# Performance work log

Measured on AMD Instinct MI355X. Metric: run time of the kernel, lower is better.

## Reference

```python
import jax, jax.numpy as jnp
import numpy as np

N_EMBED = 1024
N_HEAD = 16
SEQ = 2048
BATCH = 2


def setup_inputs() -> dict:
    key = jax.random.key(0)
    ks = jax.random.split(key, 5)
    scale_in = 1.0 / np.sqrt(N_EMBED)
    x = jax.random.normal(ks[0], (BATCH, SEQ, N_EMBED), dtype=jnp.float32)
    # attn_proj: Linear(n_embed, 3*n_embed); stored as [in, out] so y = x @ W + b
    W_qkv = jax.random.normal(ks[1], (N_EMBED, 3 * N_EMBED), dtype=jnp.float32) * scale_in
    b_qkv = jax.random.normal(ks[2], (3 * N_EMBED,), dtype=jnp.float32) * 0.01
    # fin_proj: Linear(n_embed, n_embed)
    W_out = jax.random.normal(ks[3], (N_EMBED, N_EMBED), dtype=jnp.float32) * scale_in
    b_out = jax.random.normal(ks[4], (N_EMBED,), dtype=jnp.float32) * 0.01
    return {"x": x, "W_qkv": W_qkv, "b_qkv": b_qkv, "W_out": W_out, "b_out": b_out}


def reference(x, W_qkv, b_qkv, W_out, b_out):
    B, S, D = x.shape
    H = N_HEAD
    hd = D // H
    qkv = x @ W_qkv + b_qkv  # [B, S, 3D]
    q, k, v = jnp.split(qkv, 3, axis=-1)
    # [B, H, S, hd]
    q = q.reshape(B, S, H, hd).transpose(0, 2, 1, 3)
    k = k.reshape(B, S, H, hd).transpose(0, 2, 1, 3)
    v = v.reshape(B, S, H, hd).transpose(0, 2, 1, 3)
    scores = jnp.einsum("bhqd,bhkd->bhqk", q, k) * (1.0 / np.sqrt(hd))
    causal = jnp.tril(jnp.ones((S, S), dtype=bool))  # lower-triangular mask
    scores = jnp.where(causal[None, None], scores, -jnp.inf)
    probs = jax.nn.softmax(scores, axis=-1)
    # dropout is identity in eval mode (inference reference)
    attn = jnp.einsum("bhqk,bhkd->bhqd", probs, v)  # [B, H, S, hd]
    attn = attn.transpose(0, 2, 1, 3).reshape(B, S, D)
    return attn @ W_out + b_out
```

## Files before the change

### kernel.cpp

```cpp
#include <hip/hip_runtime.h>

typedef short bf16x8 __attribute__((ext_vector_type(8)));
typedef short bf16x4 __attribute__((ext_vector_type(4)));
typedef float f32x4 __attribute__((ext_vector_type(4)));
typedef int i32x4 __attribute__((ext_vector_type(4)));
typedef int i32x2 __attribute__((ext_vector_type(2)));

#define MFMA16x16x32(a, b, c) __builtin_amdgcn_mfma_f32_16x16x32_bf16(a, b, c, 0, 0, 0)
#define TRR(dst, a) asm volatile("ds_read_b64_tr_b16 %0, %1" : "=v"(dst) : "v"(a))

__device__ __forceinline__ unsigned short f2bf(float f) {
  union { float f; unsigned u; } v; v.f = f;
  unsigned u = v.u + 0x7FFFu + ((v.u >> 16) & 1u);
  return (unsigned short)(u >> 16);
}

__device__ __forceinline__ unsigned cvtpk(float lo, float hi) {
  unsigned r;
  asm("v_cvt_pk_bf16_f32 %0, %1, %2" : "=v"(r) : "v"(lo), "v"(hi));
  return r;
}

__device__ __forceinline__ float max3f(float a, float b, float c) {
  float d;
  asm("v_max3_f32 %0, %1, %2, %3" : "=v"(d) : "v"(a), "v"(b), "v"(c));
  return d;
}

__device__ __forceinline__ void gload16(const void* g, void* l) {
  __builtin_amdgcn_global_load_lds((const __attribute__((address_space(1))) void*)g,
                                   (__attribute__((address_space(3))) void*)l, 16, 0, 0);
}

__device__ __forceinline__ unsigned ldsoff(const void* p) {
  return (unsigned)(unsigned long long)(const __attribute__((address_space(3))) void*)p;
}

__global__ __launch_bounds__(256) void conv_bf16(const float* __restrict__ in,
                                                 unsigned short* __restrict__ out, int n8) {
  int i = blockIdx.x * 256 + threadIdx.x;
  if (i >= n8) return;
  const float4* p = reinterpret_cast<const float4*>(in + (long)i * 8);
  float4 a = p[0], b = p[1];
  i32x4 o;
  o[0] = cvtpk(a.x, a.y); o[1] = cvtpk(a.z, a.w);
  o[2] = cvtpk(b.x, b.y); o[3] = cvtpk(b.z, b.w);
  *reinterpret_cast<i32x4*>(out + (long)i * 8) = o;
}

__global__ __launch_bounds__(256) void trans_f32_bf16(const float* __restrict__ W,
                                                      unsigned short* __restrict__ Wt,
                                                      int K, int N) {
  __shared__ float tile[32][33];
  int n0 = blockIdx.x << 5, k0 = blockIdx.y << 5;
  int tx = threadIdx.x, ty = threadIdx.y;
#pragma unroll
  for (int i = 0; i < 32; i += 8)
    tile[ty + i][tx] = W[(long)(k0 + ty + i) * N + n0 + tx];
  __syncthreads();
#pragma unroll
  for (int i = 0; i < 32; i += 8)
    Wt[(long)(n0 + ty + i) * K + k0 + tx] = f2bf(tile[tx][ty + i]);
}

template <int BF16OUT>
__global__ __launch_bounds__(256) void gemm_bt(const unsigned short* __restrict__ A,
                                               const unsigned short* __restrict__ Bt,
                                               const float* __restrict__ bias,
                                               void* __restrict__ Cv,
                                               int M, int N, int K) {
  __shared__ __align__(128) unsigned short As[8192];
  __shared__ __align__(128) unsigned short Bs[8192];
  int t = threadIdx.x;
  int w = t >> 6, l = t & 63;
  int g = l >> 4, m16 = l & 15;
  int wr = w >> 1, wc = w & 1;
  int nwg = gridDim.x * gridDim.y;
  int f = blockIdx.y * gridDim.x + blockIdx.x;
  int q8 = nwg >> 3;
  int s = (f & 7) * q8 + (f >> 3);
  int bx = s % gridDim.x, by = s / gridDim.x;
  long am0 = (long)by << 7;
  long bn0 = (long)bx << 7;
  f32x4 acc[4][4];
#pragma unroll
  for (int i = 0; i < 4; ++i)
#pragma unroll
    for (int j = 0; j < 4; ++j) acc[i][j] = (f32x4){0.f, 0.f, 0.f, 0.f};

  for (int k0 = 0; k0 < K; k0 += 64) {
#pragma unroll
    for (int i = 0; i < 4; ++i) {
      int seg = i * 4 + w;
      int flat = (seg << 9) + (l << 3);
      int r_ = flat >> 6, c_ = flat & 63;
      gload16(A + (am0 + r_) * K + k0 + c_, &As[seg << 9]);
      gload16(Bt + (bn0 + r_) * K + k0 + c_, &Bs[seg << 9]);
    }
    asm volatile("s_waitcnt vmcnt(0)" ::: "memory");
    __syncthreads();
#pragma unroll
    for (int kk = 0; kk < 2; ++kk) {
      bf16x8 af[4], bfr[4];
#pragma unroll
      for (int im = 0; im < 4; ++im)
        af[im] = *(const bf16x8*)&As[((wr << 6) + (im << 4) + m16) * 64 + (kk << 5) + (g << 3)];
#pragma unroll
      for (int in = 0; in < 4; ++in)
        bfr[in] = *(const bf16x8*)&Bs[((wc << 6) + (in << 4) + m16) * 64 + (kk << 5) + (g << 3)];
      __builtin_amdgcn_s_setprio(1);
#pragma unroll
      for (int im = 0; im < 4; ++im)
#pragma unroll
        for (int in = 0; in < 4; ++in)
          acc[im][in] = MFMA16x16x32(af[im], bfr[in], acc[im][in]);
      __builtin_amdgcn_s_setprio(0);
    }
    __syncthreads();
  }

#pragma unroll
  for (int im = 0; im < 4; ++im) {
#pragma unroll
    for (int in = 0; in < 4; ++in) {
      long col = bn0 + (wc << 6) + (in << 4) + m16;
      float bval = bias[col];
#pragma unroll
      for (int r = 0; r < 4; ++r) {
        long row = am0 + (wr << 6) + (im << 4) + (g << 2) + r;
        float v = acc[im][in][r] + bval;
        if (BF16OUT)
          ((unsigned short*)Cv)[row * N + col] = f2bf(v);
        else
          ((float*)Cv)[row * N + col] = v;
      }
    }
  }
}

__global__ __launch_bounds__(256, 3) void attn_fwd(const unsigned short* __restrict__ qkv,
                                                   unsigned short* __restrict__ out) {
  const int D3 = 3072;
  const float C1 = 0.18033688f;
  const float THR = 11.5415603f;
  __shared__ __align__(128) unsigned short Ks[8192];
  __shared__ __align__(128) unsigned short Vs[8192];
  int b = blockIdx.x >> 4, h = blockIdx.x & 15;
  int yy = blockIdx.y;
  int qt = (yy & 1) ? (31 - (yy >> 1)) : (yy >> 1);
  int t = threadIdx.x;
  int w = t >> 6, l = t & 63;
  int g = l >> 4, m16 = l & 15;
  long base = (long)b * 2048 * D3;
  const unsigned short* kbase = qkv + base + 1024 + h * 64;
  const unsigned short* vbase = qkv + base + 2048 + h * 64;

  int l8 = l >> 3, sc = l & 7;
  int kof = (w * 8 + l8) * D3 + ((sc ^ l8) << 3);
  int vof = ((w * 8 + l8) * 4 + (sc >> 1)) * D3 + ((sc & 1) << 3);
  const f32x4 zero4 = (f32x4){0.f, 0.f, 0.f, 0.f};

  int qrow = (qt << 6) + (w << 4) + m16;
  const unsigned short* qp = qkv + base + (long)qrow * D3 + h * 64;
  bf16x8 qf0 = *(const bf16x8*)(qp + g * 8);
  bf16x8 qf1 = *(const bf16x8*)(qp + 32 + g * 8);

  f32x4 O[4];
#pragma unroll
  for (int d = 0; d < 4; ++d) O[d] = zero4;
  f32x4 lsv = zero4;
  float m2 = -1e30f;
  int nt = (qt >> 1) + 1;

  for (int ss = 0; ss < nt; ++ss) {
    long off = (long)ss * 128 * D3;
#pragma unroll
    for (int i = 0; i < 4; ++i) {
      gload16(kbase + off + kof + i * 32 * D3, &Ks[(i << 11) + (w << 9)]);
      gload16(vbase + off + vof + (i << 4), &Vs[(i << 11) + (w << 9)]);
    }
    asm volatile("s_waitcnt vmcnt(0)" ::: "memory");
    __syncthreads();

    unsigned va = ldsoff(&Vs[0]) + (g << 7) + (m16 << 3);
    bf16x4 tLo[4][4], tHi[4][4];
#pragma unroll
    for (int G = 0; G < 4; ++G)
#pragma unroll
      for (int d = 0; d < 4; ++d) {
        unsigned a = va + (G << 10) + (d << 12);
        TRR(tLo[G][d], a);
        TRR(tHi[G][d], a + 512);
      }
    const char* kbuf = (const char*)&Ks[0];
    int swz = m16 & 7;
    f32x4 st[8];
    __builtin_amdgcn_s_setprio(1);
#pragma unroll
    for (int T = 0; T < 8; ++T) {
      const char* rp = kbuf + (((T << 4) + m16) << 7);
      bf16x8 kf0 = *(const bf16x8*)(rp + ((g ^ swz) << 4));
      bf16x8 kf1 = *(const bf16x8*)(rp + (((4 + g) ^ swz) << 4));
      st[T] = MFMA16x16x32(kf0, qf0, zero4);
      st[T] = MFMA16x16x32(kf1, qf1, st[T]);
    }
    __builtin_amdgcn_s_setprio(0);

    if (ss == nt - 1) {
      int rq = qrow - (ss << 7);
#pragma unroll
      for (int T = 0; T < 8; ++T)
#pragma unroll
        for (int r = 0; r < 4; ++r)
          if ((T << 4) + (g << 2) + r > rq) st[T][r] = -3e38f;
    }
    float tm[8];
#pragma unroll
    for (int T = 0; T < 8; ++T)
      tm[T] = max3f(fmaxf(st[T][0], st[T][1]), st[T][2], st[T][3]);
    float u0 = max3f(tm[0], tm[1], tm[2]);
    float u1 = max3f(tm[3], tm[4], tm[5]);
    float tmax = max3f(u0, u1, fmaxf(tm[6], tm[7]));
    tmax = fmaxf(tmax, __shfl_xor(tmax, 16));
    tmax = fmaxf(tmax, __shfl_xor(tmax, 32));
    float tsc2 = tmax * C1;
    bool skip = __all(tsc2 <= m2 + THR);
    float mnew2 = skip ? m2 : fmaxf(m2, tsc2);
    float p[8][4];
    f32x4 ts4 = zero4;
#pragma unroll
    for (int T = 0; T < 8; ++T)
#pragma unroll
      for (int r = 0; r < 4; ++r) {
        float e = __builtin_amdgcn_exp2f(fmaf(st[T][r], C1, -mnew2));
        p[T][r] = e;
        ts4[r] += e;
      }
    if (!skip) {
      float alpha = __builtin_amdgcn_exp2f(m2 - mnew2);
      lsv *= alpha;
#pragma unroll
      for (int d = 0; d < 4; ++d) O[d] *= alpha;
      m2 = mnew2;
    }
    lsv += ts4;

    bf16x8 pb[4];
#pragma unroll
    for (int G = 0; G < 4; ++G) {
      i32x4 wv;
      wv[0] = cvtpk(p[2 * G][0], p[2 * G][1]);
      wv[1] = cvtpk(p[2 * G][2], p[2 * G][3]);
      wv[2] = cvtpk(p[2 * G + 1][0], p[2 * G + 1][1]);
      wv[3] = cvtpk(p[2 * G + 1][2], p[2 * G + 1][3]);
      pb[G] = __builtin_bit_cast(bf16x8, wv);
    }

    asm volatile("s_waitcnt lgkmcnt(0)" ::: "memory");
    __builtin_amdgcn_sched_barrier(0);

    __builtin_amdgcn_s_setprio(1);
#pragma unroll
    for (int d = 0; d < 4; ++d)
#pragma unroll
      for (int G = 0; G < 4; ++G) {
        bf16x8 vf = __builtin_shufflevector(tLo[G][d], tHi[G][d], 0, 1, 2, 3, 4, 5, 6, 7);
        O[d] = MFMA16x16x32(vf, pb[G], O[d]);
      }
    __builtin_amdgcn_s_setprio(0);
    __syncthreads();
  }

  float s = (lsv[0] + lsv[1]) + (lsv[2] + lsv[3]);
  s += __shfl_xor(s, 16);
  s += __shfl_xor(s, 32);
  float inv = 1.0f / s;
  unsigned short* op = out + (long)(b * 2048 + qrow) * 1024 + h * 64;
#pragma unroll
  for (int d = 0; d < 4; ++d) {
    i32x2 pk;
    pk[0] = (int)cvtpk(O[d][0] * inv, O[d][1] * inv);
    pk[1] = (int)cvtpk(O[d][2] * inv, O[d][3] * inv);
    *reinterpret_cast<i32x2*>(op + (d << 4) + (g << 2)) = pk;
  }
}

extern "C" void kernel_launch(void* const* d_in, const int* in_sizes, int n_in,
                              void* d_out, int out_size, void* d_ws, size_t ws_size,
                              hipStream_t stream) {
  const float* x     = (const float*)d_in[0];
  const float* W_qkv = (const float*)d_in[1];
  const float* b_qkv = (const float*)d_in[2];
  const float* W_out = (const float*)d_in[3];
  const float* b_out = (const float*)d_in[4];

  char* ws = (char*)d_ws;
  unsigned short* xb    = (unsigned short*)ws;
  unsigned short* wqkvT = (unsigned short*)(ws + (8l << 20));
  unsigned short* woutT = (unsigned short*)(ws + (14l << 20));
  unsigned short* qkv   = (unsigned short*)(ws + (16l << 20));

  conv_bf16<<<2048, 256, 0, stream>>>(x, xb, 524288);
  trans_f32_bf16<<<dim3(96, 32), dim3(32, 8), 0, stream>>>(W_qkv, wqkvT, 1024, 3072);
  trans_f32_bf16<<<dim3(32, 32), dim3(32, 8), 0, stream>>>(W_out, woutT, 1024, 1024);
  gemm_bt<1><<<dim3(24, 32), 256, 0, stream>>>(xb, wqkvT, b_qkv, (void*)qkv, 4096, 3072, 1024);
  attn_fwd<<<dim3(32, 32), 256, 0, stream>>>(qkv, xb);
  gemm_bt<0><<<dim3(8, 32), 256, 0, stream>>>(xb, woutT, b_out, d_out, 4096, 1024, 1024);
}
```

Baseline: 121.7 us.

## Double-buffer K/V tiles in attention and shrink KV tile to 64 rows

The attention kernel now splits LDS into two 64-row K/V buffers. It prefetches the next tile with async global-to-LDS loads while computing on the current one, and drops the trailing barrier. The KV step shrinks from 128 to 64 rows, so the causal tail wastes fewer masked columns, at the cost of twice as many loop iterations and barriers. The V layout and transposed-read addressing are reworked to match the smaller tile.

```diff
diff --git a/kernel.cpp b/kernel.cpp
--- a/kernel.cpp
+++ b/kernel.cpp
@@ -143,8 +143,8 @@
   const int D3 = 3072;
   const float C1 = 0.18033688f;
   const float THR = 11.5415603f;
-  __shared__ __align__(128) unsigned short Ks[8192];
-  __shared__ __align__(128) unsigned short Vs[8192];
+  __shared__ __align__(128) unsigned short Ks[2][4096];
+  __shared__ __align__(128) unsigned short Vs[2][4096];
   int b = blockIdx.x >> 4, h = blockIdx.x & 15;
   int yy = blockIdx.y;
   int qt = (yy & 1) ? (31 - (yy >> 1)) : (yy >> 1);
@@ -157,7 +157,8 @@
 
   int l8 = l >> 3, sc = l & 7;
   int kof = (w * 8 + l8) * D3 + ((sc ^ l8) << 3);
-  int vof = ((w * 8 + l8) * 4 + (sc >> 1)) * D3 + ((sc & 1) << 3);
+  int s0 = w * 8 + l8;
+  int vof = ((s0 & 15) * 4 + (sc >> 1)) * D3 + ((s0 >> 4) << 4) + ((sc & 1) << 3);
   const f32x4 zero4 = (f32x4){0.f, 0.f, 0.f, 0.f};
 
   int qrow = (qt << 6) + (w << 4) + m16;
@@ -170,34 +171,41 @@
   for (int d = 0; d < 4; ++d) O[d] = zero4;
   f32x4 lsv = zero4;
   float m2 = -1e30f;
-  int nt = (qt >> 1) + 1;
-
+  int nt = qt + 1;
+
+  gload16(kbase + kof, &Ks[0][w << 9]);
+  gload16(kbase + 32 * D3 + kof, &Ks[0][2048 + (w << 9)]);
+  gload16(vbase + vof, &Vs[0][w << 9]);
+  gload16(vbase + vof + 32, &Vs[0][2048 + (w << 9)]);
+
+  int buf = 0;
   for (int ss = 0; ss < nt; ++ss) {
-    long off = (long)ss * 128 * D3;
-#pragma unroll
-    for (int i = 0; i < 4; ++i) {
-      gload16(kbase + off + kof + i * 32 * D3, &Ks[(i << 11) + (w << 9)]);
-      gload16(vbase + off + vof + (i << 4), &Vs[(i << 11) + (w << 9)]);
-    }
     asm volatile("s_waitcnt vmcnt(0)" ::: "memory");
     __syncthreads();
-
-    unsigned va = ldsoff(&Vs[0]) + (g << 7) + (m16 << 3);
-    bf16x4 tLo[4][4], tHi[4][4];
-#pragma unroll
-    for (int G = 0; G < 4; ++G)
-#pragma unroll
-      for (int d = 0; d < 4; ++d) {
-        unsigned a = va + (G << 10) + (d << 12);
-        TRR(tLo[G][d], a);
-        TRR(tHi[G][d], a + 512);
-      }
-    const char* kbuf = (const char*)&Ks[0];
+    if (ss + 1 < nt) {
+      long off = (long)(ss + 1) * 64 * D3;
+      gload16(kbase + off + kof, &Ks[buf ^ 1][w << 9]);
+      gload16(kbase + off + 32 * D3 + kof, &Ks[buf ^ 1][2048 + (w << 9)]);
+      gload16(vbase + off + vof, &Vs[buf ^ 1][w << 9]);
+      gload16(vbase + off + vof + 32, &Vs[buf ^ 1][2048 + (w << 9)]);
+    }
+
+    unsigned va = ldsoff(&Vs[buf][0]) + (g << 7) + (m16 << 3);
+    bf16x4 t0[4], t1[4], t2[4], t3[4];
+#pragma unroll
+    for (int d = 0; d < 4; ++d) {
+      unsigned a = va + (d << 11);
+      TRR(t0[d], a);
+      TRR(t1[d], a + 512);
+      TRR(t2[d], a + 1024);
+      TRR(t3[d], a + 1536);
+    }
+    const char* kbuf = (const char*)&Ks[buf][0];
     int swz = m16 & 7;
-    f32x4 st[8];
+    f32x4 st[4];
     __builtin_amdgcn_s_setprio(1);
 #pragma unroll
-    for (int T = 0; T < 8; ++T) {
+    for (int T = 0; T < 4; ++T) {
       const char* rp = kbuf + (((T << 4) + m16) << 7);
       bf16x8 kf0 = *(const bf16x8*)(rp + ((g ^ swz) << 4));
       bf16x8 kf1 = *(const bf16x8*)(rp + (((4 + g) ^ swz) << 4));
@@ -207,29 +215,27 @@
     __builtin_amdgcn_s_setprio(0);
 
     if (ss == nt - 1) {
-      int rq = qrow - (ss << 7);
-#pragma unroll
-      for (int T = 0; T < 8; ++T)
+      int rq = qrow - (ss << 6);
+#pragma unroll
+      for (int T = 0; T < 4; ++T)
 #pragma unroll
         for (int r = 0; r < 4; ++r)
           if ((T << 4) + (g << 2) + r > rq) st[T][r] = -3e38f;
     }
-    float tm[8];
-#pragma unroll
-    for (int T = 0; T < 8; ++T)
+    float tm[4];
+#pragma unroll
+    for (int T = 0; T < 4; ++T)
       tm[T] = max3f(fmaxf(st[T][0], st[T][1]), st[T][2], st[T][3]);
-    float u0 = max3f(tm[0], tm[1], tm[2]);
-    float u1 = max3f(tm[3], tm[4], tm[5]);
-    float tmax = max3f(u0, u1, fmaxf(tm[6], tm[7]));
+    float tmax = fmaxf(max3f(tm[0], tm[1], tm[2]), tm[3]);
     tmax = fmaxf(tmax, __shfl_xor(tmax, 16));
     tmax = fmaxf(tmax, __shfl_xor(tmax, 32));
     float tsc2 = tmax * C1;
     bool skip = __all(tsc2 <= m2 + THR);
     float mnew2 = skip ? m2 : fmaxf(m2, tsc2);
-    float p[8][4];
+    float p[4][4];
     f32x4 ts4 = zero4;
 #pragma unroll
-    for (int T = 0; T < 8; ++T)
+    for (int T = 0; T < 4; ++T)
 #pragma unroll
       for (int r = 0; r < 4; ++r) {
         float e = __builtin_amdgcn_exp2f(fmaf(st[T][r], C1, -mnew2));
@@ -245,30 +251,31 @@
     }
     lsv += ts4;
 
-    bf16x8 pb[4];
-#pragma unroll
-    for (int G = 0; G < 4; ++G) {
-      i32x4 wv;
-      wv[0] = cvtpk(p[2 * G][0], p[2 * G][1]);
-      wv[1] = cvtpk(p[2 * G][2], p[2 * G][3]);
-      wv[2] = cvtpk(p[2 * G + 1][0], p[2 * G + 1][1]);
-      wv[3] = cvtpk(p[2 * G + 1][2], p[2 * G + 1][3]);
-      pb[G] = __builtin_bit_cast(bf16x8, wv);
-    }
+    i32x4 w0, w1;
+    w0[0] = cvtpk(p[0][0], p[0][1]); w0[1] = cvtpk(p[0][2], p[0][3]);
+    w0[2] = cvtpk(p[1][0], p[1][1]); w0[3] = cvtpk(p[1][2], p[1][3]);
+    w1[0] = cvtpk(p[2][0], p[2][1]); w1[1] = cvtpk(p[2][2], p[2][3]);
+    w1[2] = cvtpk(p[3][0], p[3][1]); w1[3] = cvtpk(p[3][2], p[3][3]);
+    bf16x8 pb0 = __builtin_bit_cast(bf16x8, w0);
+    bf16x8 pb1 = __builtin_bit_cast(bf16x8, w1);
 
     asm volatile("s_waitcnt lgkmcnt(0)" ::: "memory");
     __builtin_amdgcn_sched_barrier(0);
 
+    bf16x8 vfA[4], vfB[4];
+#pragma unroll
+    for (int d = 0; d < 4; ++d) {
+      vfA[d] = __builtin_shufflevector(t0[d], t1[d], 0, 1, 2, 3, 4, 5, 6, 7);
+      vfB[d] = __builtin_shufflevector(t2[d], t3[d], 0, 1, 2, 3, 4, 5, 6, 7);
+    }
     __builtin_amdgcn_s_setprio(1);
 #pragma unroll
-    for (int d = 0; d < 4; ++d)
-#pragma unroll
-      for (int G = 0; G < 4; ++G) {
-        bf16x8 vf = __builtin_shufflevector(tLo[G][d], tHi[G][d], 0, 1, 2, 3, 4, 5, 6, 7);
-        O[d] = MFMA16x16x32(vf, pb[G], O[d]);
-      }
+    for (int d = 0; d < 4; ++d) {
+      O[d] = MFMA16x16x32(vfA[d], pb0, O[d]);
+      O[d] = MFMA16x16x32(vfB[d], pb1, O[d]);
+    }
     __builtin_amdgcn_s_setprio(0);
-    __syncthreads();
+    buf ^= 1;
   }
 
   float s = (lsv[0] + lsv[1]) + (lsv[2] + lsv[3]);
```

Measured after the change: 118.0 us. 3.0% less time.
